# Performance work log

Measured on AMD Instinct MI355X. Metric: run time of the kernel, lower is better.

## Reference

```python
import jax, jax.numpy as jnp
import numpy as np
from jax import lax

BN_EPS = 1e-5
LEAKY_RATE = 0.1
SPECTRAL_RADIUS = 0.99


def _bn_eval(x, gamma, beta, mean, var):
    # x: (B, F, ...); params: (F,) broadcast over trailing dims
    shape = (1, -1) + (1,) * (x.ndim - 2)
    inv = gamma.reshape(shape) / jnp.sqrt(var.reshape(shape) + BN_EPS)
    return (x - mean.reshape(shape)) * inv + beta.reshape(shape)


def setup_inputs() -> dict:
    key = jax.random.key(0)
    ks = jax.random.split(key, 12)
    B, C, T, F, H, NCLS = 32, 72, 1000, 64, 512, 3
    x = jax.random.normal(ks[0], (B, 1, C, T), dtype=jnp.float32)
    w_temp = jax.random.normal(ks[1], (F, 1, 1, 5), dtype=jnp.float32) * 0.1
    bn1_gamma = jnp.ones((F,), jnp.float32)
    bn1_beta = jnp.zeros((F,), jnp.float32)
    bn1_mean = jax.random.normal(ks[2], (F,), dtype=jnp.float32) * 0.1
    bn1_var = jax.random.uniform(ks[3], (F,), dtype=jnp.float32) + 0.5
    w_spatial = jax.random.normal(ks[4], (F, C), dtype=jnp.float32) * 0.1
    bn2_gamma = jnp.ones((F,), jnp.float32)
    bn2_beta = jnp.zeros((F,), jnp.float32)
    bn2_mean = jax.random.normal(ks[5], (F,), dtype=jnp.float32) * 0.1
    bn2_var = jax.random.uniform(ks[6], (F,), dtype=jnp.float32) + 0.5
    w_in = jax.random.normal(ks[7], (H, F), dtype=jnp.float32) * (1.0 / np.sqrt(F))
    b_in = jax.random.normal(ks[8], (H,), dtype=jnp.float32) * 0.1
    # reservoir weight: uniform(-0.5, 0.5) scaled to spectral norm = 0.99 (frozen in torch)
    W = jax.random.uniform(ks[9], (H, H), dtype=jnp.float32, minval=-0.5, maxval=0.5)
    W = W * (SPECTRAL_RADIUS / jnp.linalg.norm(W, ord=2))
    w_cls = jax.random.normal(ks[10], (NCLS, H), dtype=jnp.float32) * (1.0 / np.sqrt(H))
    b_cls = jax.random.normal(ks[11], (NCLS,), dtype=jnp.float32) * 0.1
    return dict(x=x, w_temp=w_temp, bn1_gamma=bn1_gamma, bn1_beta=bn1_beta,
                bn1_mean=bn1_mean, bn1_var=bn1_var, w_spatial=w_spatial,
                bn2_gamma=bn2_gamma, bn2_beta=bn2_beta, bn2_mean=bn2_mean,
                bn2_var=bn2_var, w_in=w_in, b_in=b_in, W=W, w_cls=w_cls, b_cls=b_cls)


def _forward(x, w_temp, bn1_gamma, bn1_beta, bn1_mean, bn1_var, w_spatial,
             bn2_gamma, bn2_beta, bn2_mean, bn2_var, w_in, b_in, W, w_cls, b_cls):
    # temporal conv: (B,1,C,T) -> (B,F,C,T), kernel (1,5), pad (0,2)
    out = lax.conv_general_dilated(x, w_temp, window_strides=(1, 1),
                                   padding=((0, 0), (2, 2)),
                                   dimension_numbers=('NCHW', 'OIHW', 'NCHW'))
    out = jax.nn.elu(_bn_eval(out, bn1_gamma, bn1_beta, bn1_mean, bn1_var))
    # depthwise spatial conv over full channel height: (B,F,C,T) x (F,C) -> (B,F,T)
    out = jnp.einsum('bfct,fc->bft', out, w_spatial)
    out = jax.nn.elu(_bn_eval(out, bn2_gamma, bn2_beta, bn2_mean, bn2_var))
    feats = jnp.swapaxes(out, 1, 2)  # (B, T, F)
    # ESN: precompute input projection, scan the nonlinear recurrence over time
    u_in = jnp.einsum('btf,hf->bth', feats, w_in) + b_in  # (B,T,H)
    B, T, H = u_in.shape
    a = LEAKY_RATE

    def step(h, u_t):
        h_new = (1.0 - a) * h + a * jnp.tanh(u_t + h @ W.T)
        return h_new, h_new

    h0 = jnp.zeros((B, H), u_in.dtype)
    _, hs = lax.scan(step, h0, jnp.swapaxes(u_in, 0, 1))  # hs: (T,B,H)
    pooled = hs.mean(axis=0)  # mean over time (dropout is identity at eval)
    return pooled @ w_cls.T + b_cls  # (B, n_classes)


def reference(x, w_temp, bn1_gamma, bn1_beta, bn1_mean, bn1_var, w_spatial,
              bn2_gamma, bn2_beta, bn2_mean, bn2_var, w_in, b_in, W, w_cls, b_cls):
    return _forward(x, w_temp, bn1_gamma, bn1_beta, bn1_mean, bn1_var, w_spatial,
                    bn2_gamma, bn2_beta, bn2_mean, bn2_var, w_in, b_in, W, w_cls, b_cls)
```

## Files before the change

kernel.cpp:

```cpp
#include <hip/hip_runtime.h>
#include <math.h>

#define NB 32
#define NC 72
#define NT 1000
#define NF 64
#define NH 512
#define NCLS 3

#define OFF_WT      0
#define OFF_WINT    262144
#define OFF_FEATS   294912
#define OFF_POOLED  2342912
#define OFF_HX      2359296
#define WS_FLOATS   2424832

#define HIDX(k) ((k) + (((k) >> 7) << 2))

__global__ void prep_kernel(const float* __restrict__ Wm,
                            const float* __restrict__ w_in,
                            float* __restrict__ ws_f) {
  int i = blockIdx.x * 256 + threadIdx.x;
  if (i < NH * NH) {
    int j = i / NH, k = i % NH;
    ws_f[OFF_WT + k * NH + j] = Wm[i];
  }
  if (i < NH * NF) {
    int h = i / NF, f = i % NF;
    ws_f[OFF_WINT + f * NH + h] = w_in[i];
  }
  if (i < 2 * NB * NH) {
    ((unsigned long long*)(ws_f + OFF_HX))[i] = 0ull;
  }
}

__global__ __launch_bounds__(256) void frontend_kernel(
    const float* __restrict__ x, const float* __restrict__ w_temp,
    const float* __restrict__ g1, const float* __restrict__ be1,
    const float* __restrict__ m1, const float* __restrict__ v1,
    const float* __restrict__ wsp,
    const float* __restrict__ g2, const float* __restrict__ be2,
    const float* __restrict__ m2, const float* __restrict__ v2,
    float* __restrict__ feats) {
  const int b = blockIdx.y;
  const int t0 = blockIdx.x * 64;

  __shared__ float xs[NC][68];
  for (int idx = threadIdx.x; idx < NC * 68; idx += 256) {
    int c = idx / 68, tt = idx % 68;
    int tg = t0 - 2 + tt;
    xs[c][tt] = (tg >= 0 && tg < NT) ? x[(b * NC + c) * NT + tg] : 0.0f;
  }
  __syncthreads();

  const int f = threadIdx.x & 63;
  const int tq = threadIdx.x >> 6;

  const float w0 = w_temp[f * 5 + 0], w1 = w_temp[f * 5 + 1], w2 = w_temp[f * 5 + 2],
              w3 = w_temp[f * 5 + 3], w4 = w_temp[f * 5 + 4];
  const float sc1 = g1[f] * rsqrtf(v1[f] + 1e-5f);
  const float sh1 = be1[f] - m1[f] * sc1;
  const float sc2 = g2[f] * rsqrtf(v2[f] + 1e-5f);
  const float sh2 = be2[f] - m2[f] * sc2;

  for (int i = 0; i < 16; ++i) {
    const int tl = tq + 4 * i;
    const int t = t0 + tl;
    if (t >= NT) break;
    float acc = 0.0f;
    for (int c = 0; c < NC; ++c) {
      const float* xr = &xs[c][tl];
      float conv = xr[0] * w0 + xr[1] * w1 + xr[2] * w2 + xr[3] * w3 + xr[4] * w4;
      float bn = conv * sc1 + sh1;
      float e = bn > 0.0f ? bn : __expf(bn) - 1.0f;
      acc += e * wsp[f * NC + c];
    }
    float bn2 = acc * sc2 + sh2;
    float e2 = bn2 > 0.0f ? bn2 : __expf(bn2) - 1.0f;
    feats[(b * NT + t) * NF + f] = e2;
  }
}

__global__ __launch_bounds__(512, 1) void esn_scan(
    const float* __restrict__ ws_f, const float* __restrict__ b_in,
    unsigned long long* __restrict__ hx, float* __restrict__ pooled) {
  const int b = blockIdx.x & 31;
  const int m = blockIdx.x >> 5;
  const int tid = threadIdx.x;
  const int jl = tid >> 2;
  const int p = tid & 3;
  const int j = m * 128 + jl;

  const float* __restrict__ Wt = ws_f + OFF_WT;
  const float* __restrict__ w_inT = ws_f + OFF_WINT;
  const float* __restrict__ feats = ws_f + OFF_FEATS;

  __shared__ __align__(16) float h2[2][NH + 16];
  __shared__ __align__(16) float f2[2][NF];

  float w[128];
#pragma unroll
  for (int i = 0; i < 128; ++i) w[i] = Wt[(p * 128 + i) * NH + j];
#pragma unroll
  for (int i = 0; i < 128; ++i) asm volatile("" : "+v"(w[i]));
  float wu[16];
#pragma unroll
  for (int i = 0; i < 16; ++i) wu[i] = w_inT[(p * 16 + i) * NH + j];
#pragma unroll
  for (int i = 0; i < 16; ++i) asm volatile("" : "+v"(wu[i]));
  const float bias = (p == 0) ? b_in[j] : 0.0f;

  for (int i = tid; i < NH + 16; i += 512) h2[0][i] = 0.0f;
  if (tid < NF) f2[0][tid] = feats[(b * NT) * NF + tid];
  __syncthreads();

  float* hc = &h2[0][0];
  float* hb = &h2[1][0];
  float* fc = &f2[0][0];
  float* fb = &f2[1][0];

  float pool = 0.0f;
  int budget = 20000000;

#pragma unroll 1
  for (int t = 0; t < NT; ++t) {
    float acc = bias;
#pragma unroll
    for (int i = 0; i < 16; i += 4) {
      float4 fv = *(const float4*)&fc[p * 16 + i];
      acc += fv.x * wu[i] + fv.y * wu[i + 1] + fv.z * wu[i + 2] + fv.w * wu[i + 3];
    }
#pragma unroll
    for (int i = 0; i < 128; i += 4) {
      float4 hv = *(const float4*)&hc[HIDX(p * 128 + i)];
      acc += hv.x * w[i] + hv.y * w[i + 1] + hv.z * w[i + 2] + hv.w * w[i + 3];
    }
    acc += __shfl_xor(acc, 1);
    acc += __shfl_xor(acc, 2);
    const float hn = 0.9f * hc[HIDX(j)] + 0.1f * tanhf(acc);
    if (p == 0) pool += hn;
    if (t == NT - 1) break;

    unsigned long long* hxb = hx + ((t + 1) & 1) * (NB * NH) + b * NH;
    if (p == 0) {
      unsigned long long pk =
          ((unsigned long long)(unsigned)(t + 1) << 32) | (unsigned)__float_as_uint(hn);
      __hip_atomic_store(&hxb[j], pk, __ATOMIC_RELAXED, __HIP_MEMORY_SCOPE_AGENT);
      hb[HIDX(j)] = hn;
    }

    float fnext = 0.0f;
    if (tid < NF) fnext = feats[(b * NT + t + 1) * NF + tid];

    const int k = tid;
    if ((k >> 7) != m) {
      unsigned long long q;
      for (;;) {
        q = __hip_atomic_load(&hxb[k], __ATOMIC_RELAXED, __HIP_MEMORY_SCOPE_AGENT);
        if ((unsigned)(q >> 32) == (unsigned)(t + 1)) break;
        if (--budget < 0) break;
        __builtin_amdgcn_s_sleep(1);
      }
      hb[HIDX(k)] = __uint_as_float((unsigned)q);
    }
    if (tid < NF) fb[tid] = fnext;
    __syncthreads();
    { float* tp = hc; hc = hb; hb = tp; }
    { float* tp = fc; fc = fb; fb = tp; }
  }

  if (p == 0) pooled[b * NH + j] = pool * (1.0f / NT);
}

__global__ void classifier_kernel(const float* __restrict__ pooled,
                                  const float* __restrict__ w_cls,
                                  const float* __restrict__ b_cls,
                                  float* __restrict__ out) {
  const int b = blockIdx.x;
  const int lane = threadIdx.x;
  float a0 = 0.0f, a1 = 0.0f, a2 = 0.0f;
  for (int jj = lane; jj < NH; jj += 64) {
    float pv = pooled[b * NH + jj];
    a0 += pv * w_cls[0 * NH + jj];
    a1 += pv * w_cls[1 * NH + jj];
    a2 += pv * w_cls[2 * NH + jj];
  }
  for (int off = 32; off; off >>= 1) {
    a0 += __shfl_down(a0, off);
    a1 += __shfl_down(a1, off);
    a2 += __shfl_down(a2, off);
  }
  if (lane == 0) {
    out[b * NCLS + 0] = a0 + b_cls[0];
    out[b * NCLS + 1] = a1 + b_cls[1];
    out[b * NCLS + 2] = a2 + b_cls[2];
  }
}

extern "C" void kernel_launch(void* const* d_in, const int* in_sizes, int n_in,
                              void* d_out, int out_size, void* d_ws, size_t ws_size,
                              hipStream_t stream) {
  (void)in_sizes; (void)n_in; (void)out_size;
  if (ws_size < (size_t)WS_FLOATS * 4) return;

  const float* x      = (const float*)d_in[0];
  const float* w_temp = (const float*)d_in[1];
  const float* g1  = (const float*)d_in[2];
  const float* be1 = (const float*)d_in[3];
  const float* m1  = (const float*)d_in[4];
  const float* v1  = (const float*)d_in[5];
  const float* wsp = (const float*)d_in[6];
  const float* g2  = (const float*)d_in[7];
  const float* be2 = (const float*)d_in[8];
  const float* m2  = (const float*)d_in[9];
  const float* v2  = (const float*)d_in[10];
  const float* w_in  = (const float*)d_in[11];
  const float* b_in  = (const float*)d_in[12];
  const float* Wm    = (const float*)d_in[13];
  const float* w_cls = (const float*)d_in[14];
  const float* b_cls = (const float*)d_in[15];

  float* ws_f  = (float*)d_ws;
  float* feats = ws_f + OFF_FEATS;
  float* pooledp = ws_f + OFF_POOLED;
  unsigned long long* hx = (unsigned long long*)(ws_f + OFF_HX);

  prep_kernel<<<1024, 256, 0, stream>>>(Wm, w_in, ws_f);

  dim3 gfe(16, NB);
  frontend_kernel<<<gfe, 256, 0, stream>>>(x, w_temp, g1, be1, m1, v1, wsp,
                                           g2, be2, m2, v2, feats);

  esn_scan<<<128, 512, 0, stream>>>(ws_f, b_in, hx, pooledp);

  classifier_kernel<<<NB, 64, 0, stream>>>(pooledp, w_cls, b_cls, (float*)d_out);
}
```

Before: 1.942 ms.

## Restructure ESN scan thread mapping to 4 outputs per 16-lane group

Each 16-lane group now computes four hidden outputs, with each lane covering a 32-element slice of h. Every h float4 read from LDS is therefore reused across four rows held in registers, and the LDS padding is changed to HIDX2 to spread banks for the new access pattern. Weights are loaded directly from the untransposed W and w_in, so the transpose work in the prep kernel and its workspace region are removed. The cost is a longer shuffle reduction (four xor levels for each of four accumulators) and a select step for the output lane.

```diff
diff --git a/kernel.cpp b/kernel.cpp
--- a/kernel.cpp
+++ b/kernel.cpp
@@ -8,30 +8,17 @@
 #define NH 512
 #define NCLS 3
 
-#define OFF_WT      0
-#define OFF_WINT    262144
-#define OFF_FEATS   294912
-#define OFF_POOLED  2342912
-#define OFF_HX      2359296
-#define WS_FLOATS   2424832
-
-#define HIDX(k) ((k) + (((k) >> 7) << 2))
-
-__global__ void prep_kernel(const float* __restrict__ Wm,
-                            const float* __restrict__ w_in,
-                            float* __restrict__ ws_f) {
+#define OFF_FEATS   0
+#define OFF_POOLED  2048000
+#define OFF_HX      2064384
+#define WS_FLOATS   2129920
+
+#define HIDX2(k) ((k) + (((k) >> 5) << 2))
+#define HPAD (NH + 64)
+
+__global__ void prep_kernel(unsigned long long* __restrict__ hx) {
   int i = blockIdx.x * 256 + threadIdx.x;
-  if (i < NH * NH) {
-    int j = i / NH, k = i % NH;
-    ws_f[OFF_WT + k * NH + j] = Wm[i];
-  }
-  if (i < NH * NF) {
-    int h = i / NF, f = i % NF;
-    ws_f[OFF_WINT + f * NH + h] = w_in[i];
-  }
-  if (i < 2 * NB * NH) {
-    ((unsigned long long*)(ws_f + OFF_HX))[i] = 0ull;
-  }
+  if (i < 2 * NB * NH) hx[i] = 0ull;
 }
 
 __global__ __launch_bounds__(256) void frontend_kernel(
@@ -82,35 +69,46 @@
 }
 
 __global__ __launch_bounds__(512, 1) void esn_scan(
-    const float* __restrict__ ws_f, const float* __restrict__ b_in,
+    const float* __restrict__ Wm, const float* __restrict__ w_in,
+    const float* __restrict__ b_in, const float* __restrict__ feats,
     unsigned long long* __restrict__ hx, float* __restrict__ pooled) {
   const int b = blockIdx.x & 31;
   const int m = blockIdx.x >> 5;
   const int tid = threadIdx.x;
-  const int jl = tid >> 2;
-  const int p = tid & 3;
-  const int j = m * 128 + jl;
-
-  const float* __restrict__ Wt = ws_f + OFF_WT;
-  const float* __restrict__ w_inT = ws_f + OFF_WINT;
-  const float* __restrict__ feats = ws_f + OFF_FEATS;
-
-  __shared__ __align__(16) float h2[2][NH + 16];
+  const int grp = tid >> 4;
+  const int p = tid & 15;
+  const int c0 = m * 128 + grp * 4;
+
+  __shared__ __align__(16) float h2[2][HPAD];
   __shared__ __align__(16) float f2[2][NF];
 
-  float w[128];
-#pragma unroll
-  for (int i = 0; i < 128; ++i) w[i] = Wt[(p * 128 + i) * NH + j];
-#pragma unroll
-  for (int i = 0; i < 128; ++i) asm volatile("" : "+v"(w[i]));
-  float wu[16];
-#pragma unroll
-  for (int i = 0; i < 16; ++i) wu[i] = w_inT[(p * 16 + i) * NH + j];
-#pragma unroll
-  for (int i = 0; i < 16; ++i) asm volatile("" : "+v"(wu[i]));
-  const float bias = (p == 0) ? b_in[j] : 0.0f;
-
-  for (int i = tid; i < NH + 16; i += 512) h2[0][i] = 0.0f;
+  float w[4][32];
+#pragma unroll
+  for (int c = 0; c < 4; ++c)
+#pragma unroll
+    for (int i = 0; i < 32; i += 4) {
+      float4 t = *(const float4*)&Wm[(c0 + c) * NH + p * 32 + i];
+      w[c][i] = t.x; w[c][i + 1] = t.y; w[c][i + 2] = t.z; w[c][i + 3] = t.w;
+    }
+#pragma unroll
+  for (int c = 0; c < 4; ++c)
+#pragma unroll
+    for (int i = 0; i < 32; ++i) asm volatile("" : "+v"(w[c][i]));
+
+  float wu[4][4];
+#pragma unroll
+  for (int c = 0; c < 4; ++c) {
+    float4 t = *(const float4*)&w_in[(c0 + c) * NF + p * 4];
+    wu[c][0] = t.x; wu[c][1] = t.y; wu[c][2] = t.z; wu[c][3] = t.w;
+  }
+  float be[4];
+  {
+    float4 bv = *(const float4*)&b_in[c0];
+    be[0] = p == 0 ? bv.x : 0.0f; be[1] = p == 0 ? bv.y : 0.0f;
+    be[2] = p == 0 ? bv.z : 0.0f; be[3] = p == 0 ? bv.w : 0.0f;
+  }
+
+  for (int i = tid; i < HPAD; i += 512) h2[0][i] = 0.0f;
   if (tid < NF) f2[0][tid] = feats[(b * NT) * NF + tid];
   __syncthreads();
 
@@ -124,30 +122,43 @@
 
 #pragma unroll 1
   for (int t = 0; t < NT; ++t) {
-    float acc = bias;
-#pragma unroll
-    for (int i = 0; i < 16; i += 4) {
-      float4 fv = *(const float4*)&fc[p * 16 + i];
-      acc += fv.x * wu[i] + fv.y * wu[i + 1] + fv.z * wu[i + 2] + fv.w * wu[i + 3];
-    }
-#pragma unroll
-    for (int i = 0; i < 128; i += 4) {
-      float4 hv = *(const float4*)&hc[HIDX(p * 128 + i)];
-      acc += hv.x * w[i] + hv.y * w[i + 1] + hv.z * w[i + 2] + hv.w * w[i + 3];
-    }
-    acc += __shfl_xor(acc, 1);
-    acc += __shfl_xor(acc, 2);
-    const float hn = 0.9f * hc[HIDX(j)] + 0.1f * tanhf(acc);
-    if (p == 0) pool += hn;
+    float acc[4] = {be[0], be[1], be[2], be[3]};
+    {
+      float4 fv = *(const float4*)&fc[p * 4];
+#pragma unroll
+      for (int c = 0; c < 4; ++c)
+        acc[c] += fv.x * wu[c][0] + fv.y * wu[c][1] + fv.z * wu[c][2] + fv.w * wu[c][3];
+    }
+#pragma unroll
+    for (int i = 0; i < 8; ++i) {
+      float4 hv = *(const float4*)&hc[p * 36 + i * 4];
+#pragma unroll
+      for (int c = 0; c < 4; ++c)
+        acc[c] += hv.x * w[c][i * 4] + hv.y * w[c][i * 4 + 1] +
+                  hv.z * w[c][i * 4 + 2] + hv.w * w[c][i * 4 + 3];
+    }
+#pragma unroll
+    for (int c = 0; c < 4; ++c) {
+      acc[c] += __shfl_xor(acc[c], 1);
+      acc[c] += __shfl_xor(acc[c], 2);
+      acc[c] += __shfl_xor(acc[c], 4);
+      acc[c] += __shfl_xor(acc[c], 8);
+    }
+
+    unsigned long long* hxb = hx + ((t + 1) & 1) * (NB * NH) + b * NH;
+    if (p < 4) {
+      const int j = c0 + p;
+      float asel = p == 0 ? acc[0] : p == 1 ? acc[1] : p == 2 ? acc[2] : acc[3];
+      float hn = 0.9f * hc[HIDX2(j)] + 0.1f * tanhf(asel);
+      pool += hn;
+      if (t < NT - 1) {
+        unsigned long long pk =
+            ((unsigned long long)(unsigned)(t + 1) << 32) | (unsigned)__float_as_uint(hn);
+        __hip_atomic_store(&hxb[j], pk, __ATOMIC_RELAXED, __HIP_MEMORY_SCOPE_AGENT);
+        hb[HIDX2(j)] = hn;
+      }
+    }
     if (t == NT - 1) break;
-
-    unsigned long long* hxb = hx + ((t + 1) & 1) * (NB * NH) + b * NH;
-    if (p == 0) {
-      unsigned long long pk =
-          ((unsigned long long)(unsigned)(t + 1) << 32) | (unsigned)__float_as_uint(hn);
-      __hip_atomic_store(&hxb[j], pk, __ATOMIC_RELAXED, __HIP_MEMORY_SCOPE_AGENT);
-      hb[HIDX(j)] = hn;
-    }
 
     float fnext = 0.0f;
     if (tid < NF) fnext = feats[(b * NT + t + 1) * NF + tid];
@@ -161,7 +172,7 @@
         if (--budget < 0) break;
         __builtin_amdgcn_s_sleep(1);
       }
-      hb[HIDX(k)] = __uint_as_float((unsigned)q);
+      hb[HIDX2(k)] = __uint_as_float((unsigned)q);
     }
     if (tid < NF) fb[tid] = fnext;
     __syncthreads();
@@ -169,7 +180,7 @@
     { float* tp = fc; fc = fb; fb = tp; }
   }
 
-  if (p == 0) pooled[b * NH + j] = pool * (1.0f / NT);
+  if (p < 4) pooled[b * NH + c0 + p] = pool * (1.0f / NT);
 }
 
 __global__ void classifier_kernel(const float* __restrict__ pooled,
@@ -225,13 +236,13 @@
   float* pooledp = ws_f + OFF_POOLED;
   unsigned long long* hx = (unsigned long long*)(ws_f + OFF_HX);
 
-  prep_kernel<<<1024, 256, 0, stream>>>(Wm, w_in, ws_f);
+  prep_kernel<<<128, 256, 0, stream>>>(hx);
 
   dim3 gfe(16, NB);
   frontend_kernel<<<gfe, 256, 0, stream>>>(x, w_temp, g1, be1, m1, v1, wsp,
                                            g2, be2, m2, v2, feats);
 
-  esn_scan<<<128, 512, 0, stream>>>(ws_f, b_in, hx, pooledp);
+  esn_scan<<<128, 512, 0, stream>>>(Wm, w_in, b_in, feats, hx, pooledp);
 
   classifier_kernel<<<NB, 64, 0, stream>>>(pooledp, w_cls, b_cls, (float*)d_out);
 }
```

Measured after the change: 1.693 ms. -12.8%, faster.
